# Kernel tuning notes

Measured on AMD Instinct MI355X. Metric: run time of the kernel, lower is better.

The kernel has to match this reference:

```python
import jax, jax.numpy as jnp
import numpy as np

S, V_SHELL, V_GRID = 4, 90, 642   # shells, dirs/shell, grid vertices
B, F_IN, X, Y, Z = 2, 8, 12, 12, 12


def setup_inputs() -> dict:
    key = jax.random.key(0)
    k1, k2 = jax.random.split(key)
    x = jax.random.normal(k1, (B, F_IN, S * V_SHELL, X, Y, Z), dtype=jnp.float32)
    # per-shell interpolation matrices S2SH @ SH2S[:C], shape [S, V_shell, V_grid]
    W = jax.random.normal(k2, (S, V_SHELL, V_GRID), dtype=jnp.float32) * 0.05
    # shells are concatenated in order -> shell_inverse is sorted with equal counts
    shell_inverse = jnp.repeat(jnp.arange(S, dtype=jnp.int64), V_SHELL)
    return {"x": x, "W": W, "shell_inverse": shell_inverse}


def reference(x, W, shell_inverse):
    # x: [B, F, V', X, Y, Z] with V' = S * V_shell, shell_inverse sorted -> static reshape
    b, f, vp, xx, yy, zz = x.shape
    s, vs, vg = W.shape
    xs = x.reshape(b, f, s, vs, xx, yy, zz)  # per-shell gather (contiguous blocks)
    # einsum 'ijklmn,kp->ijplmn' per shell; output channel block i*F:(i+1)*F -> shell-major
    y = jnp.einsum('bfskxyz,skp->bsfpxyz', xs, W)
    return y.reshape(b, s * f, vg, xx, yy, zz)
```

## Files before the change

kernel.cpp:

```cpp
#include <hip/hip_runtime.h>
#include <cstdint>
#include <cstddef>

#define NB 2
#define NF 8
#define NS 4
#define NK 90
#define NP 642
#define NXYZ 1728
#define MT 64
#define PTILES 11
#define NG 108
#define XT_TASKS (64 * NG * 3)
#define WT_TASKS (NS * PTILES * 4 * 3)
#define GEMM_TASKS (64 * 54 * PTILES)
#define GEMM_BLOCKS (GEMM_TASKS / 4)
#define NXCD 8
#define CPX (GEMM_BLOCKS / NXCD)

typedef __attribute__((ext_vector_type(8))) __bf16 bf16x8;
typedef __attribute__((ext_vector_type(4))) float f32x4;
typedef __attribute__((ext_vector_type(4))) uint32_t u32x4;

__device__ __forceinline__ uint32_t pack2bf(float a, float b) {
    uint32_t ua = __builtin_bit_cast(uint32_t, a);
    uint32_t ub = __builtin_bit_cast(uint32_t, b);
    ua += 0x7FFFu + ((ua >> 16) & 1u);
    ub += 0x7FFFu + ((ub >> 16) & 1u);
    return (ua >> 16) | (ub & 0xFFFF0000u);
}

__global__ __launch_bounds__(256) void prep_frag(
    const float* __restrict__ x, const float* __restrict__ Wm,
    uint32_t* __restrict__ ws)
{
    const int tid  = (int)threadIdx.x;
    const int lane = tid & 63;
    const int lr = lane & 15, lg = lane >> 4;
    const int task = (int)blockIdx.x * 4 + (tid >> 6);

    float v[8];
    if (task < XT_TASKS) {
        int t = task;
        const int kk = t % 3;   t /= 3;
        const int g  = t % NG;  t /= NG;
        const int e  = t;
        const int s = e & 3, bf = e >> 2;
        const float* src = x + (size_t)bf * (NS * NK * NXYZ)
                             + (size_t)s * (NK * NXYZ) + g * 16 + lr;
        #pragma unroll
        for (int j = 0; j < 8; ++j) {
            const int k = kk * 32 + lg * 8 + j;
            v[j] = (k < NK) ? src[(size_t)k * NXYZ] : 0.f;
        }
    } else {
        int t = task - XT_TASKS;
        const int kk = t % 3;      t /= 3;
        const int ni = t % 4;      t /= 4;
        const int pt = t % PTILES; t /= PTILES;
        const int s  = t;
        const int p = pt * MT + ni * 16 + lr;
        const float* src = Wm + (size_t)s * (NK * NP) + p;
        #pragma unroll
        for (int j = 0; j < 8; ++j) {
            const int k = kk * 32 + lg * 8 + j;
            v[j] = (k < NK && p < NP) ? src[(size_t)k * NP] : 0.f;
        }
    }
    u32x4 u;
    u.x = pack2bf(v[0], v[1]);
    u.y = pack2bf(v[2], v[3]);
    u.z = pack2bf(v[4], v[5]);
    u.w = pack2bf(v[6], v[7]);
    *(u32x4*)((char*)ws + (size_t)task * 1024 + lane * 16) = u;
}

__global__ __launch_bounds__(256, 4) void gemm_frag(
    const uint32_t* __restrict__ ws, float* __restrict__ y)
{
    const int tid  = (int)threadIdx.x;
    const int lane = tid & 63;
    const int lr = lane & 15, lg = lane >> 4;

    const int i = (int)blockIdx.x;
    const int orig = (i % NXCD) * CPX + i / NXCD;
    int t = orig * 4 + (tid >> 6);
    const int pt  = t % PTILES; t /= PTILES;
    const int n32 = t % 54;     t /= 54;
    const int e   = t;
    const int s = e & 3, bf = e >> 2;

    const char* base  = (const char*)ws + (size_t)lane * 16;
    const char* xbase = base + (size_t)((e * NG + n32 * 2) * 3) * 1024;
    const char* abase = base + (size_t)(XT_TASKS + ((s * PTILES + pt) * 4) * 3) * 1024;

    bf16x8 bfr[2][3], afr[4][3];
    #pragma unroll
    for (int mi = 0; mi < 2; ++mi)
        #pragma unroll
        for (int kk = 0; kk < 3; ++kk)
            bfr[mi][kk] = *(const bf16x8*)(xbase + (mi * 3 + kk) * 1024);
    #pragma unroll
    for (int ni = 0; ni < 4; ++ni)
        #pragma unroll
        for (int kk = 0; kk < 3; ++kk)
            afr[ni][kk] = *(const bf16x8*)(abase + (ni * 3 + kk) * 1024);

    f32x4 acc[2][4];
    #pragma unroll
    for (int mi = 0; mi < 2; ++mi)
        #pragma unroll
        for (int ni = 0; ni < 4; ++ni)
            acc[mi][ni] = (f32x4){0.f, 0.f, 0.f, 0.f};

    #pragma unroll
    for (int kk = 0; kk < 3; ++kk)
        #pragma unroll
        for (int mi = 0; mi < 2; ++mi)
            #pragma unroll
            for (int ni = 0; ni < 4; ++ni)
                acc[mi][ni] = __builtin_amdgcn_mfma_f32_16x16x32_bf16(
                    bfr[mi][kk], afr[ni][kk], acc[mi][ni], 0, 0, 0);

    const int b = bf >> 3, f = bf & 7;
    const size_t chan = (size_t)b * (NS * NF) + (size_t)s * NF + f;
    float* ybase = y + chan * ((size_t)NP * NXYZ) + n32 * 32 + lg * 4;
    #pragma unroll
    for (int ni = 0; ni < 4; ++ni) {
        const int p = pt * MT + ni * 16 + lr;
        if (p < NP) {
            float* dst = ybase + (size_t)p * NXYZ;
            *(f32x4*)dst = acc[0][ni];
            *(f32x4*)(dst + 16) = acc[1][ni];
        }
    }
}

#define NT 96
#define NTILES 18
#define KP 96
#define ROWB (KP * 2)

__global__ __launch_bounds__(192, 4) void interp_fallback(
    const float* __restrict__ x, const float* __restrict__ Wm,
    float* __restrict__ y)
{
    __shared__ __align__(16) char As[MT * ROWB];
    __shared__ __align__(16) char Bs[NT * ROWB];

    int blk = (int)blockIdx.x;
    const int nt = blk % NTILES; blk /= NTILES;
    const int f  = blk % NF;     blk /= NF;
    const int s  = blk % NS;     blk /= NS;
    const int b  = blk;
    const int tid = (int)threadIdx.x;
    const int n0 = nt * NT;

    {
        const int c  = tid % NT;
        const int kh = tid / NT;
        const float* xp = x + (((size_t)b * NF + f) * (NS * NK) + (size_t)s * NK) * NXYZ
                            + n0 + c;
        const int cs = (c & 7) << 4;
        #pragma unroll
        for (int kk = 0; kk < 48; kk += 8) {
            const int kb = kh * 48 + kk;
            float v[8];
            #pragma unroll
            for (int j = 0; j < 8; ++j) {
                const int k = kb + j;
                v[j] = (k < NK) ? xp[(size_t)k * NXYZ] : 0.f;
            }
            u32x4 u;
            u.x = pack2bf(v[0], v[1]); u.y = pack2bf(v[2], v[3]);
            u.z = pack2bf(v[4], v[5]); u.w = pack2bf(v[6], v[7]);
            *(u32x4*)(Bs + ((c * ROWB + kb * 2) ^ cs)) = u;
        }
    }

    const int lane = tid & 63;
    const int w  = tid / 64;
    const int lr = lane & 15;
    const int lg = lane >> 4;
    const int ls = (lr & 7) << 4;
    const size_t chan = (size_t)b * (NS * NF) + (size_t)s * NF + f;
    float* ybase = y + chan * ((size_t)NP * NXYZ);
    const int xyzbase = n0 + w * 32 + lg * 4;
    const int ar = tid & 63;
    const int akc = tid >> 6;
    const int ars = (ar & 7) << 4;

    for (int pt = 0; pt < PTILES; ++pt) {
        const int p0 = pt * MT;
        __syncthreads();
        {
            const int p = p0 + ar;
            const bool pv = (p < NP);
            const float* wp = Wm + (size_t)s * NK * NP + p;
            #pragma unroll
            for (int kk = 0; kk < 32; kk += 8) {
                const int kb = akc * 32 + kk;
                float v[8];
                #pragma unroll
                for (int j = 0; j < 8; ++j) {
                    const int k = kb + j;
                    v[j] = (pv && (k < NK)) ? wp[(size_t)k * NP] : 0.f;
                }
                u32x4 u;
                u.x = pack2bf(v[0], v[1]); u.y = pack2bf(v[2], v[3]);
                u.z = pack2bf(v[4], v[5]); u.w = pack2bf(v[6], v[7]);
                *(u32x4*)(As + ((ar * ROWB + kb * 2) ^ ars)) = u;
            }
        }
        __syncthreads();

        f32x4 acc[2][4];
        #pragma unroll
        for (int mi = 0; mi < 2; ++mi)
            #pragma unroll
            for (int ni = 0; ni < 4; ++ni)
                acc[mi][ni] = (f32x4){0.f, 0.f, 0.f, 0.f};

        #pragma unroll
        for (int kk = 0; kk < 3; ++kk) {
            const int kbyte = kk * 64 + lg * 16;
            bf16x8 bxyz[2], ap[4];
            #pragma unroll
            for (int mi = 0; mi < 2; ++mi) {
                const int row = w * 32 + mi * 16 + lr;
                bxyz[mi] = *(const bf16x8*)(Bs + ((row * ROWB + kbyte) ^ ls));
            }
            #pragma unroll
            for (int ni = 0; ni < 4; ++ni) {
                const int row = ni * 16 + lr;
                ap[ni] = *(const bf16x8*)(As + ((row * ROWB + kbyte) ^ ls));
            }
            #pragma unroll
            for (int mi = 0; mi < 2; ++mi)
                #pragma unroll
                for (int ni = 0; ni < 4; ++ni)
                    acc[mi][ni] = __builtin_amdgcn_mfma_f32_16x16x32_bf16(
                        bxyz[mi], ap[ni], acc[mi][ni], 0, 0, 0);
        }

        #pragma unroll
        for (int ni = 0; ni < 4; ++ni) {
            const int p = p0 + ni * 16 + lr;
            if (p < NP) {
                float* dst = ybase + (size_t)p * NXYZ + xyzbase;
                *(f32x4*)dst = acc[0][ni];
                *(f32x4*)(dst + 16) = acc[1][ni];
            }
        }
    }
}

extern "C" void kernel_launch(void* const* d_in, const int* in_sizes, int n_in,
                              void* d_out, int out_size, void* d_ws, size_t ws_size,
                              hipStream_t stream) {
    (void)in_sizes; (void)n_in; (void)out_size;
    const float* x  = (const float*)d_in[0];
    const float* Wm = (const float*)d_in[1];
    float* y = (float*)d_out;

    const size_t ws_need = (size_t)(XT_TASKS + WT_TASKS) * 1024;
    if (ws_size >= ws_need) {
        prep_frag<<<(XT_TASKS + WT_TASKS) / 4, 256, 0, stream>>>(x, Wm, (uint32_t*)d_ws);
        gemm_frag<<<GEMM_BLOCKS, 256, 0, stream>>>((const uint32_t*)d_ws, y);
    } else {
        interp_fallback<<<NB * NS * NF * NTILES, 192, 0, stream>>>(x, Wm, y);
    }
}
```

Before: 80.90 us.

## Process three N-tiles per wave to reuse W fragments with double-buffered X loads

Each wave now keeps its loaded W (A) fragments in registers and reuses them across three consecutive 32-column output chunks instead of one. X fragments for the next chunk are prefetched into a second register set while the current chunk computes and stores. Blocks shrink to 3 waves, the grid shrinks threefold, and the launch bounds change to (192,3). This cuts redundant W fragment loads and block launch overhead, at the cost of higher register pressure and fewer waves in flight.

```diff
diff --git a/kernel.cpp b/kernel.cpp
--- a/kernel.cpp
+++ b/kernel.cpp
@@ -13,8 +13,8 @@
 #define NG 108
 #define XT_TASKS (64 * NG * 3)
 #define WT_TASKS (NS * PTILES * 4 * 3)
-#define GEMM_TASKS (64 * 54 * PTILES)
-#define GEMM_BLOCKS (GEMM_TASKS / 4)
+#define NWG 18
+#define GEMM_BLOCKS (64 * PTILES * 6)
 #define NXCD 8
 #define CPX (GEMM_BLOCKS / NXCD)
 
@@ -75,65 +75,80 @@
     *(u32x4*)((char*)ws + (size_t)task * 1024 + lane * 16) = u;
 }
 
-__global__ __launch_bounds__(256, 4) void gemm_frag(
+__global__ __launch_bounds__(192, 3) void gemm_frag3n(
     const uint32_t* __restrict__ ws, float* __restrict__ y)
 {
     const int tid  = (int)threadIdx.x;
     const int lane = tid & 63;
     const int lr = lane & 15, lg = lane >> 4;
+    const int w    = tid >> 6;
 
     const int i = (int)blockIdx.x;
     const int orig = (i % NXCD) * CPX + i / NXCD;
-    int t = orig * 4 + (tid >> 6);
-    const int pt  = t % PTILES; t /= PTILES;
-    const int n32 = t % 54;     t /= 54;
-    const int e   = t;
+    const int sext = orig % 6;
+    const int pt   = (orig / 6) % PTILES;
+    const int e    = orig / 66;
+    const int wg   = sext * 3 + w;
     const int s = e & 3, bf = e >> 2;
 
     const char* base  = (const char*)ws + (size_t)lane * 16;
-    const char* xbase = base + (size_t)((e * NG + n32 * 2) * 3) * 1024;
+    const char* xbase = base + (size_t)((e * NG + wg * 6) * 3) * 1024;
     const char* abase = base + (size_t)(XT_TASKS + ((s * PTILES + pt) * 4) * 3) * 1024;
 
-    bf16x8 bfr[2][3], afr[4][3];
-    #pragma unroll
-    for (int mi = 0; mi < 2; ++mi)
-        #pragma unroll
-        for (int kk = 0; kk < 3; ++kk)
-            bfr[mi][kk] = *(const bf16x8*)(xbase + (mi * 3 + kk) * 1024);
+    bf16x8 afr[4][3];
     #pragma unroll
     for (int ni = 0; ni < 4; ++ni)
         #pragma unroll
         for (int kk = 0; kk < 3; ++kk)
             afr[ni][kk] = *(const bf16x8*)(abase + (ni * 3 + kk) * 1024);
 
-    f32x4 acc[2][4];
-    #pragma unroll
-    for (int mi = 0; mi < 2; ++mi)
-        #pragma unroll
-        for (int ni = 0; ni < 4; ++ni)
-            acc[mi][ni] = (f32x4){0.f, 0.f, 0.f, 0.f};
-
-    #pragma unroll
-    for (int kk = 0; kk < 3; ++kk)
-        #pragma unroll
-        for (int mi = 0; mi < 2; ++mi)
-            #pragma unroll
-            for (int ni = 0; ni < 4; ++ni)
-                acc[mi][ni] = __builtin_amdgcn_mfma_f32_16x16x32_bf16(
-                    bfr[mi][kk], afr[ni][kk], acc[mi][ni], 0, 0, 0);
-
     const int b = bf >> 3, f = bf & 7;
     const size_t chan = (size_t)b * (NS * NF) + (size_t)s * NF + f;
-    float* ybase = y + chan * ((size_t)NP * NXYZ) + n32 * 32 + lg * 4;
-    #pragma unroll
-    for (int ni = 0; ni < 4; ++ni) {
-        const int p = pt * MT + ni * 16 + lr;
-        if (p < NP) {
-            float* dst = ybase + (size_t)p * NXYZ;
-            *(f32x4*)dst = acc[0][ni];
-            *(f32x4*)(dst + 16) = acc[1][ni];
-        }
-    }
+    float* ybase = y + chan * ((size_t)NP * NXYZ) + wg * 96 + lg * 4;
+
+    bf16x8 bA[6], bB[6];
+
+    #pragma unroll
+    for (int q = 0; q < 6; ++q)
+        bA[q] = *(const bf16x8*)(xbase + q * 1024);
+
+#define COMPUTE_STORE(BSET, H)                                              \
+    {                                                                       \
+        f32x4 acc[2][4];                                                    \
+        _Pragma("unroll")                                                   \
+        for (int kk = 0; kk < 3; ++kk)                                      \
+            _Pragma("unroll")                                               \
+            for (int mi = 0; mi < 2; ++mi)                                  \
+                _Pragma("unroll")                                           \
+                for (int ni = 0; ni < 4; ++ni)                              \
+                    acc[mi][ni] = __builtin_amdgcn_mfma_f32_16x16x32_bf16(  \
+                        BSET[mi * 3 + kk], afr[ni][kk],                     \
+                        kk ? acc[mi][ni] : (f32x4){0.f, 0.f, 0.f, 0.f},     \
+                        0, 0, 0);                                           \
+        float* yh = ybase + (H) * 32;                                       \
+        _Pragma("unroll")                                                   \
+        for (int ni = 0; ni < 4; ++ni) {                                    \
+            const int p = pt * MT + ni * 16 + lr;                           \
+            if (p < NP) {                                                   \
+                float* dst = yh + (size_t)p * NXYZ;                         \
+                *(f32x4*)dst = acc[0][ni];                                  \
+                *(f32x4*)(dst + 16) = acc[1][ni];                           \
+            }                                                               \
+        }                                                                   \
+    }
+
+    #pragma unroll
+    for (int q = 0; q < 6; ++q)
+        bB[q] = *(const bf16x8*)(xbase + (6 + q) * 1024);
+    COMPUTE_STORE(bA, 0)
+
+    #pragma unroll
+    for (int q = 0; q < 6; ++q)
+        bA[q] = *(const bf16x8*)(xbase + (12 + q) * 1024);
+    COMPUTE_STORE(bB, 1)
+
+    COMPUTE_STORE(bA, 2)
+#undef COMPUTE_STORE
 }
 
 #define NT 96
@@ -266,7 +281,7 @@
     const size_t ws_need = (size_t)(XT_TASKS + WT_TASKS) * 1024;
     if (ws_size >= ws_need) {
         prep_frag<<<(XT_TASKS + WT_TASKS) / 4, 256, 0, stream>>>(x, Wm, (uint32_t*)d_ws);
-        gemm_frag<<<GEMM_BLOCKS, 256, 0, stream>>>((const uint32_t*)d_ws, y);
+        gemm_frag3n<<<GEMM_BLOCKS, 192, 0, stream>>>((const uint32_t*)d_ws, y);
     } else {
         interp_fallback<<<NB * NS * NF * NTILES, 192, 0, stream>>>(x, Wm, y);
     }
```

Result: faster. 73.97 us, median of 2 (-8.6%).
